# Performance work log

Measured on AMD Instinct MI355X. Metric: run time of the kernel, lower is better.

Reference implementation:

```python
import jax, jax.numpy as jnp
import numpy as np

N, E = 50000, 600000
IN_DIM, HID, HYP = 384, 128, 256
NUM_LAYERS = 3
TAU = 0.5
ALPHA = 0.1
EPS = 1e-10


def setup_inputs() -> dict:
    keys = jax.random.split(jax.random.key(0), 10)
    x = jax.random.normal(keys[0], (N, IN_DIM), dtype=jnp.float32)
    edge_index = jax.random.randint(keys[1], (2, E), 0, N, dtype=jnp.int32)
    gumbel_u = jax.random.uniform(keys[2], (N, HYP), dtype=jnp.float32, minval=1e-6, maxval=1.0 - 1e-6)
    # parameters (xavier-ish scaling)
    w_feat = jax.random.normal(keys[3], (IN_DIM, HID), dtype=jnp.float32) * np.float32(1.0 / np.sqrt(IN_DIM))
    b_feat = jnp.zeros((HID,), jnp.float32)
    w_hyper = jax.random.normal(keys[4], (HID, HYP), dtype=jnp.float32) * np.float32(np.sqrt(2.0 / (HID + HYP)))
    w_vis = jax.random.normal(keys[5], (HID, HID), dtype=jnp.float32) * np.float32(1.0 / np.sqrt(HID))
    b_vis = jnp.zeros((HID,), jnp.float32)
    w_txt = jax.random.normal(keys[6], (HID, HID), dtype=jnp.float32) * np.float32(1.0 / np.sqrt(HID))
    b_txt = jnp.zeros((HID,), jnp.float32)
    return {"x": x, "edge_index": edge_index, "gumbel_u": gumbel_u,
            "w_feat": w_feat, "b_feat": b_feat, "w_hyper": w_hyper,
            "w_vis": w_vis, "b_vis": b_vis, "w_txt": w_txt, "b_txt": b_txt}


def reference(x, edge_index, gumbel_u, w_feat, b_feat, w_hyper, w_vis, b_vis, w_txt, b_txt):
    src, dst = edge_index[0], edge_index[1]
    # LGConv gcn_norm (no self loops): deg from in-edges, norm = d_src^-1/2 * d_dst^-1/2
    deg = jax.ops.segment_sum(jnp.ones((E,), x.dtype), dst, num_segments=N)
    dinv = jnp.where(deg > 0, jnp.where(deg > 0, deg, 1.0) ** -0.5, 0.0)
    ew = dinv[src] * dinv[dst]  # [E]

    x_emb = x @ w_feat + b_feat  # [N, HID] (dropout p=0 / eval: identity)

    # stacked LightGCN propagation, mean over (num_layers+1) layer outputs
    acc = x_emb
    cur = x_emb
    for _ in range(NUM_LAYERS):
        cur = jax.ops.segment_sum(cur[src] * ew[:, None], dst, num_segments=N)
        acc = acc + cur
    local = acc / jnp.asarray(NUM_LAYERS + 1, x.dtype)

    # HGNN: gumbel-softmax soft assignment + two dense matmuls
    logits = x_emb @ w_hyper  # [N, HYP]
    g = -jnp.log(-jnp.log(gumbel_u + EPS) + EPS)
    Hm = jax.nn.softmax((logits + g) / TAU, axis=1)  # [N, HYP]
    lat = Hm.T @ x_emb            # [HYP, HID]
    hyper_out = Hm @ lat          # [N, HID]

    # F.normalize(p=2, dim=1) with eps clamp 1e-12
    nrm = jnp.maximum(jnp.linalg.norm(hyper_out, axis=1, keepdims=True), 1e-12)
    final = local + ALPHA * (hyper_out / nrm)

    x_vision = jax.nn.relu(final @ w_vis + b_vis)
    x_text = jax.nn.relu(final @ w_txt + b_txt)
    return final, x_vision, x_text
```

## Files before the change

kernel.cpp:

```cpp
#include <hip/hip_runtime.h>
#include <math.h>

#define N_NODES 50000
#define E_EDGES 600000
#define IN_DIM  384
#define HID     128
#define HYP     256

#define SCAN_NB ((N_NODES + 255) / 256)
#define EMB_NB  (N_NODES / 16)
#define DEG_NB  ((E_EDGES + 127) / 128)

typedef __attribute__((ext_vector_type(8))) short bf16x8;
typedef __attribute__((ext_vector_type(4))) float f32x4;
typedef _Float16 f16x4 __attribute__((ext_vector_type(4)));
typedef _Float16 f16x8 __attribute__((ext_vector_type(8)));

__device__ __forceinline__ unsigned short f2bf(float f) {
    unsigned u = __builtin_bit_cast(unsigned, f);
    u = (u + 0x7FFFu + ((u >> 16) & 1u)) >> 16;
    return (unsigned short)u;
}

__device__ __forceinline__ bf16x8 cvt8(float4 p, float4 q) {
    bf16x8 a;
    a[0] = (short)f2bf(p.x); a[1] = (short)f2bf(p.y);
    a[2] = (short)f2bf(p.z); a[3] = (short)f2bf(p.w);
    a[4] = (short)f2bf(q.x); a[5] = (short)f2bf(q.y);
    a[6] = (short)f2bf(q.z); a[7] = (short)f2bf(q.w);
    return a;
}

__device__ __forceinline__ bf16x8 cvt8h(f16x8 h) {
    bf16x8 a;
#pragma unroll
    for (int i = 0; i < 8; ++i) a[i] = (short)f2bf((float)h[i]);
    return a;
}


__global__ __launch_bounds__(256) void k_scan1(const int* __restrict__ deg, int* __restrict__ bsum) {
    __shared__ int sh[256];
    int tid = threadIdx.x;
    int i = blockIdx.x * 256 + tid;
    sh[tid] = (i < N_NODES) ? deg[i] : 0;
    __syncthreads();
#pragma unroll
    for (int off = 128; off > 0; off >>= 1) {
        if (tid < off) sh[tid] += sh[tid + off];
        __syncthreads();
    }
    if (tid == 0) bsum[blockIdx.x] = sh[0];
}

__global__ __launch_bounds__(256) void k_scan2(const int* __restrict__ bsum, int* __restrict__ bbase,
                                               int* __restrict__ row_start) {
    __shared__ int sh[256];
    int tid = threadIdx.x;
    int v = (tid < SCAN_NB) ? bsum[tid] : 0;
    sh[tid] = v;
    __syncthreads();
#pragma unroll
    for (int off = 1; off < 256; off <<= 1) {
        int t = (tid >= off) ? sh[tid - off] : 0;
        __syncthreads();
        sh[tid] += t;
        __syncthreads();
    }
    if (tid < SCAN_NB) bbase[tid] = sh[tid] - v;
    if (tid == 0) row_start[N_NODES] = E_EDGES;
}

__global__ __launch_bounds__(256) void k_scan3(const int* __restrict__ deg, const int* __restrict__ bbase,
                                               int* __restrict__ row_start, float* __restrict__ dinv) {
    __shared__ int sh[256];
    int tid = threadIdx.x;
    int i = blockIdx.x * 256 + tid;
    int d = (i < N_NODES) ? deg[i] : 0;
    sh[tid] = d;
    __syncthreads();
#pragma unroll
    for (int off = 1; off < 256; off <<= 1) {
        int t = (tid >= off) ? sh[tid - off] : 0;
        __syncthreads();
        sh[tid] += t;
        __syncthreads();
    }
    if (i < N_NODES) {
        row_start[i] = sh[tid] - d + bbase[blockIdx.x];
        dinv[i] = (d > 0) ? rsqrtf((float)d) : 0.0f;
    }
}

__global__ void k_fill(const int* __restrict__ src, const int* __restrict__ dst,
                       const int* __restrict__ row_start, int* __restrict__ cnt,
                       const float* __restrict__ dinv, int2* __restrict__ csr_sw) {
    int i = blockIdx.x * blockDim.x + threadIdx.x;
    if (i < E_EDGES) {
        int d = dst[i], s = src[i];
        int pos = row_start[d] + atomicAdd(&cnt[d], 1);
        csr_sw[pos] = make_int2(s, __float_as_int(dinv[s] * dinv[d]));
    }
}


__global__ __launch_bounds__(256) void k_cvt_all(const float* __restrict__ wf, const float* __restrict__ wh,
                                                 const float* __restrict__ wv, const float* __restrict__ wt,
                                                 unsigned short* __restrict__ wfT, unsigned short* __restrict__ whT,
                                                 unsigned short* __restrict__ wvT, unsigned short* __restrict__ wtT) {
    int i = blockIdx.x * 256 + threadIdx.x;
    if (i < 49152) {
        int r = i >> 7, c = i & 127;
        wfT[(size_t)c * IN_DIM + r] = f2bf(wf[i]);
    } else if (i < 49152 + 32768) {
        int j = i - 49152;
        int r = j >> 8, c = j & 255;
        whT[(size_t)c * HID + r] = f2bf(wh[j]);
    } else if (i < 49152 + 32768 + 16384) {
        int j = i - 81920;
        int r = j >> 7, c = j & 127;
        wvT[(size_t)c * HID + r] = f2bf(wv[j]);
    } else {
        int j = i - 98304;
        int r = j >> 7, c = j & 127;
        wtT[(size_t)c * HID + r] = f2bf(wt[j]);
    }
}


__global__ __launch_bounds__(128) void k_embdeg(const float* __restrict__ x, const unsigned short* __restrict__ wfT,
                                                const float* __restrict__ bf_, _Float16* __restrict__ x_embh,
                                                const int* __restrict__ dst, int* __restrict__ deg) {
    int b = blockIdx.x;
    if (b >= EMB_NB) {
        int i = (b - EMB_NB) * 128 + threadIdx.x;
        if (i < E_EDGES) atomicAdd(&deg[dst[i]], 1);
        return;
    }
    __shared__ float red[16 * HID];
    int tid = threadIdx.x;
    int wid = tid >> 6;
    int lane = tid & 63;
    int l16 = lane & 15, quad = lane >> 4;
    int m0 = b * 16;
    const float* xrow = x + (size_t)(m0 + l16) * IN_DIM + wid * 192 + quad * 8;
    float4 P[6], Q[6];
#pragma unroll
    for (int kt = 0; kt < 6; ++kt) {
        P[kt] = *reinterpret_cast<const float4*>(xrow + kt * 32);
        Q[kt] = *reinterpret_cast<const float4*>(xrow + kt * 32 + 4);
    }
    f32x4 acc[8];
#pragma unroll
    for (int nt = 0; nt < 8; ++nt) acc[nt] = (f32x4){0.f, 0.f, 0.f, 0.f};
#pragma unroll
    for (int kt = 0; kt < 6; ++kt) {
        bf16x8 a = cvt8(P[kt], Q[kt]);
#pragma unroll
        for (int nt = 0; nt < 8; ++nt) {
            bf16x8 bfr = *reinterpret_cast<const bf16x8*>(
                &wfT[(size_t)(nt * 16 + l16) * IN_DIM + wid * 192 + kt * 32 + quad * 8]);
            acc[nt] = __builtin_amdgcn_mfma_f32_16x16x32_bf16(a, bfr, acc[nt], 0, 0, 0);
        }
    }
    if (wid == 1) {
#pragma unroll
        for (int nt = 0; nt < 8; ++nt)
#pragma unroll
            for (int r = 0; r < 4; ++r)
                red[(quad * 4 + r) * HID + nt * 16 + l16] = acc[nt][r];
    }
    __syncthreads();
    if (wid == 0) {
#pragma unroll
        for (int nt = 0; nt < 8; ++nt) {
            int col = nt * 16 + l16;
            float bias = bf_[col];
#pragma unroll
            for (int r = 0; r < 4; ++r) {
                int lrow = quad * 4 + r;
                float v = acc[nt][r] + red[lrow * HID + col] + bias;
                x_embh[(size_t)(m0 + lrow) * HID + col] = (_Float16)v;
            }
        }
    }
}


__device__ __forceinline__ void fma4h(float4& a, const f16x4 v, float s) {
    a.x = fmaf((float)v.x, s, a.x);
    a.y = fmaf((float)v.y, s, a.y);
    a.z = fmaf((float)v.z, s, a.z);
    a.w = fmaf((float)v.w, s, a.w);
}

template <int INIT, int LAST>
__global__ __launch_bounds__(256) void k_prop(const _Float16* __restrict__ curh, _Float16* __restrict__ nxth,
                                              float* __restrict__ accb,
                                              const int* __restrict__ row_start,
                                              const int2* __restrict__ csr_sw) {
    int tid = threadIdx.x;
    int n = blockIdx.x * 8 + (tid >> 5);
    int c4 = (tid & 31) * 4;
    int s = row_start[n];
    int e = row_start[n + 1];
    float4 a[8];
#pragma unroll
    for (int k = 0; k < 8; ++k) a[k] = (float4){0.f, 0.f, 0.f, 0.f};
    for (int i = s; i < e; i += 8) {
        int2 pk[8];
        float wk[8];
#pragma unroll
        for (int k = 0; k < 8; ++k) {
            int j = i + k;
            pk[k] = csr_sw[(j < e) ? j : s];
            wk[k] = (j < e) ? __int_as_float(pk[k].y) : 0.0f;
        }
        f16x4 v[8];
#pragma unroll
        for (int k = 0; k < 8; ++k)
            v[k] = *reinterpret_cast<const f16x4*>(&curh[(size_t)pk[k].x * HID + c4]);
#pragma unroll
        for (int k = 0; k < 8; ++k) fma4h(a[k], v[k], wk[k]);
    }
    a[0].x += a[1].x; a[0].y += a[1].y; a[0].z += a[1].z; a[0].w += a[1].w;
    a[2].x += a[3].x; a[2].y += a[3].y; a[2].z += a[3].z; a[2].w += a[3].w;
    a[4].x += a[5].x; a[4].y += a[5].y; a[4].z += a[5].z; a[4].w += a[5].w;
    a[6].x += a[7].x; a[6].y += a[7].y; a[6].z += a[7].z; a[6].w += a[7].w;
    a[0].x += a[2].x; a[0].y += a[2].y; a[0].z += a[2].z; a[0].w += a[2].w;
    a[4].x += a[6].x; a[4].y += a[6].y; a[4].z += a[6].z; a[4].w += a[6].w;
    a[0].x += a[4].x; a[0].y += a[4].y; a[0].z += a[4].z; a[0].w += a[4].w;
    size_t o = (size_t)n * HID + c4;
    if (!LAST) {
        f16x4 oh;
        oh.x = (_Float16)a[0].x; oh.y = (_Float16)a[0].y;
        oh.z = (_Float16)a[0].z; oh.w = (_Float16)a[0].w;
        *reinterpret_cast<f16x4*>(&nxth[o]) = oh;
    }
    float4 ac;
    if (INIT) {
        f16x4 bh = *reinterpret_cast<const f16x4*>(&curh[o]);
        ac = make_float4((float)bh.x, (float)bh.y, (float)bh.z, (float)bh.w);
    } else {
        ac = *reinterpret_cast<const float4*>(&accb[o]);
    }
    ac.x += a[0].x; ac.y += a[0].y; ac.z += a[0].z; ac.w += a[0].w;
    *reinterpret_cast<float4*>(&accb[o]) = ac;
}


__global__ __launch_bounds__(64) void k_soft(const _Float16* __restrict__ x_embh,
                                             const unsigned short* __restrict__ whT,
                                             const float* __restrict__ gu, _Float16* __restrict__ Hmh) {
    int lane = threadIdx.x & 63;
    int l16 = lane & 15, quad = lane >> 4;
    int m0 = blockIdx.x * 16;
    const _Float16* xrow = x_embh + (size_t)(m0 + l16) * HID + quad * 8;
    f32x4 acc[16];
#pragma unroll
    for (int nt = 0; nt < 16; ++nt) acc[nt] = (f32x4){0.f, 0.f, 0.f, 0.f};
#pragma unroll
    for (int kt = 0; kt < HID / 32; ++kt) {
        f16x8 h = *reinterpret_cast<const f16x8*>(xrow + kt * 32);
        bf16x8 a = cvt8h(h);
#pragma unroll
        for (int nt = 0; nt < 16; ++nt) {
            bf16x8 b = *reinterpret_cast<const bf16x8*>(&whT[(size_t)(nt * 16 + l16) * HID + kt * 32 + quad * 8]);
            acc[nt] = __builtin_amdgcn_mfma_f32_16x16x32_bf16(a, b, acc[nt], 0, 0, 0);
        }
    }
#pragma unroll
    for (int nt = 0; nt < 16; ++nt) {
        int col = nt * 16 + l16;
#pragma unroll
        for (int r = 0; r < 4; ++r) {
            int row = m0 + quad * 4 + r;
            float u = gu[(size_t)row * HYP + col];
            float g = -logf(-logf(u + 1e-10f) + 1e-10f);
            acc[nt][r] = (acc[nt][r] + g) * 2.0f;
        }
    }
    float mx[4] = {-3.4e38f, -3.4e38f, -3.4e38f, -3.4e38f};
#pragma unroll
    for (int nt = 0; nt < 16; ++nt)
#pragma unroll
        for (int r = 0; r < 4; ++r) mx[r] = fmaxf(mx[r], acc[nt][r]);
#pragma unroll
    for (int r = 0; r < 4; ++r) {
        mx[r] = fmaxf(mx[r], __shfl_xor(mx[r], 1));
        mx[r] = fmaxf(mx[r], __shfl_xor(mx[r], 2));
        mx[r] = fmaxf(mx[r], __shfl_xor(mx[r], 4));
        mx[r] = fmaxf(mx[r], __shfl_xor(mx[r], 8));
    }
    float sm[4] = {0.f, 0.f, 0.f, 0.f};
#pragma unroll
    for (int nt = 0; nt < 16; ++nt)
#pragma unroll
        for (int r = 0; r < 4; ++r) {
            float e = __expf(acc[nt][r] - mx[r]);
            acc[nt][r] = e;
            sm[r] += e;
        }
#pragma unroll
    for (int r = 0; r < 4; ++r) {
        sm[r] += __shfl_xor(sm[r], 1);
        sm[r] += __shfl_xor(sm[r], 2);
        sm[r] += __shfl_xor(sm[r], 4);
        sm[r] += __shfl_xor(sm[r], 8);
        sm[r] = 1.0f / sm[r];
    }
#pragma unroll
    for (int nt = 0; nt < 16; ++nt) {
        int col = nt * 16 + l16;
#pragma unroll
        for (int r = 0; r < 4; ++r)
            Hmh[(size_t)(m0 + quad * 4 + r) * HYP + col] = (_Float16)(acc[nt][r] * sm[r]);
    }
}


#define LAT_KC 384

__global__ __launch_bounds__(256) void k_lat(const _Float16* __restrict__ Hmh, const _Float16* __restrict__ x_embh,
                                             float* __restrict__ part) {
    int htile = blockIdx.x & 1;
    int kc = blockIdx.x >> 1;
    const int chunk = (N_NODES + LAT_KC - 1) / LAT_KC;
    int start = kc * chunk;
    int end = min(N_NODES, start + chunk);
    int nn = end - start;
    int tid = threadIdx.x;
    int lh = (tid & 15) * 8;
    int d = (tid >> 4) * 8;
    const _Float16* __restrict__ hp = Hmh + (size_t)start * HYP + htile * 128 + lh;
    const _Float16* __restrict__ xp = x_embh + (size_t)start * HID + d;
    float acc[8][8];
#pragma unroll
    for (int i = 0; i < 8; ++i)
#pragma unroll
        for (int j = 0; j < 8; ++j) acc[i][j] = 0.f;
#pragma unroll 2
    for (int n = 0; n < nn; ++n) {
        f16x8 ah = *reinterpret_cast<const f16x8*>(hp);
        f16x8 bh = *reinterpret_cast<const f16x8*>(xp);
        float av[8], bv[8];
#pragma unroll
        for (int i = 0; i < 8; ++i) { av[i] = (float)ah[i]; bv[i] = (float)bh[i]; }
#pragma unroll
        for (int i = 0; i < 8; ++i)
#pragma unroll
            for (int j = 0; j < 8; ++j) acc[i][j] = fmaf(av[i], bv[j], acc[i][j]);
        hp += HYP;
        xp += HID;
    }
    float* __restrict__ pp = part + (size_t)blockIdx.x * (128 * 128) + (size_t)lh * 128 + d;
#pragma unroll
    for (int i = 0; i < 8; ++i) {
        float4 v0 = {acc[i][0], acc[i][1], acc[i][2], acc[i][3]};
        float4 v1 = {acc[i][4], acc[i][5], acc[i][6], acc[i][7]};
        *reinterpret_cast<float4*>(pp + i * 128) = v0;
        *reinterpret_cast<float4*>(pp + i * 128 + 4) = v1;
    }
}


__global__ __launch_bounds__(256) void k_lat_red(const float* __restrict__ part, unsigned short* __restrict__ latT) {
    int idx = blockIdx.x * 256 + threadIdx.x;
    int d = idx & 127;
    int h = idx >> 7;
    int htile = h >> 7;
    int lh = h & 127;
    const float* __restrict__ p0 = part + (size_t)htile * (128 * 128) + (size_t)lh * 128 + d;
    const size_t kstride = (size_t)2 * 128 * 128;
    float s0 = 0.f, s1 = 0.f, s2 = 0.f, s3 = 0.f;
#pragma unroll 4
    for (int k = 0; k < LAT_KC; k += 4) {
        s0 += p0[(size_t)k * kstride];
        s1 += p0[(size_t)(k + 1) * kstride];
        s2 += p0[(size_t)(k + 2) * kstride];
        s3 += p0[(size_t)(k + 3) * kstride];
    }
    latT[(size_t)d * HYP + h] = f2bf((s0 + s1) + (s2 + s3));
}


__global__ __launch_bounds__(64) void k_tail(const _Float16* __restrict__ Hmh, const unsigned short* __restrict__ latT,
                                             const float* __restrict__ accb,
                                             const unsigned short* __restrict__ wvT, const float* __restrict__ bv,
                                             const unsigned short* __restrict__ wtT, const float* __restrict__ bt,
                                             float* __restrict__ out_final, float* __restrict__ out_vis,
                                             float* __restrict__ out_txt) {
    __shared__ unsigned short fl[16 * HID];
    int lane = threadIdx.x & 63;
    int l16 = lane & 15, quad = lane >> 4;
    int m0 = blockIdx.x * 16;
    const _Float16* hrow = Hmh + (size_t)(m0 + l16) * HYP + quad * 8;
    f32x4 acc[8];
#pragma unroll
    for (int nt = 0; nt < 8; ++nt) acc[nt] = (f32x4){0.f, 0.f, 0.f, 0.f};
#pragma unroll
    for (int kt = 0; kt < HYP / 32; ++kt) {
        f16x8 h = *reinterpret_cast<const f16x8*>(hrow + kt * 32);
        bf16x8 a = cvt8h(h);
#pragma unroll
        for (int nt = 0; nt < 8; ++nt) {
            bf16x8 b = *reinterpret_cast<const bf16x8*>(&latT[(size_t)(nt * 16 + l16) * HYP + kt * 32 + quad * 8]);
            acc[nt] = __builtin_amdgcn_mfma_f32_16x16x32_bf16(a, b, acc[nt], 0, 0, 0);
        }
    }
    float ss[4] = {0.f, 0.f, 0.f, 0.f};
#pragma unroll
    for (int nt = 0; nt < 8; ++nt)
#pragma unroll
        for (int r = 0; r < 4; ++r) ss[r] = fmaf(acc[nt][r], acc[nt][r], ss[r]);
#pragma unroll
    for (int r = 0; r < 4; ++r) {
        ss[r] += __shfl_xor(ss[r], 1);
        ss[r] += __shfl_xor(ss[r], 2);
        ss[r] += __shfl_xor(ss[r], 4);
        ss[r] += __shfl_xor(ss[r], 8);
        ss[r] = 1.0f / fmaxf(sqrtf(ss[r]), 1e-12f);
    }
#pragma unroll
    for (int nt = 0; nt < 8; ++nt) {
        int col = nt * 16 + l16;
#pragma unroll
        for (int r = 0; r < 4; ++r) {
            int lrow = quad * 4 + r;
            size_t o = (size_t)(m0 + lrow) * HID + col;
            float f = accb[o] * 0.25f + 0.1f * (acc[nt][r] * ss[r]);
            out_final[o] = f;
            fl[lrow * HID + col] = f2bf(f);
        }
    }
    __syncthreads();
    f32x4 av[8], at4[8];
#pragma unroll
    for (int nt = 0; nt < 8; ++nt) {
        av[nt] = (f32x4){0.f, 0.f, 0.f, 0.f};
        at4[nt] = (f32x4){0.f, 0.f, 0.f, 0.f};
    }
#pragma unroll
    for (int kt = 0; kt < HID / 32; ++kt) {
        bf16x8 a = *reinterpret_cast<const bf16x8*>(&fl[l16 * HID + kt * 32 + quad * 8]);
#pragma unroll
        for (int nt = 0; nt < 8; ++nt) {
            bf16x8 b1 = *reinterpret_cast<const bf16x8*>(&wvT[(size_t)(nt * 16 + l16) * HID + kt * 32 + quad * 8]);
            bf16x8 b2 = *reinterpret_cast<const bf16x8*>(&wtT[(size_t)(nt * 16 + l16) * HID + kt * 32 + quad * 8]);
            av[nt] = __builtin_amdgcn_mfma_f32_16x16x32_bf16(a, b1, av[nt], 0, 0, 0);
            at4[nt] = __builtin_amdgcn_mfma_f32_16x16x32_bf16(a, b2, at4[nt], 0, 0, 0);
        }
    }
#pragma unroll
    for (int nt = 0; nt < 8; ++nt) {
        int col = nt * 16 + l16;
        float b1 = bv[col], b2 = bt[col];
#pragma unroll
        for (int r = 0; r < 4; ++r) {
            size_t o = (size_t)(m0 + quad * 4 + r) * HID + col;
            out_vis[o] = fmaxf(av[nt][r] + b1, 0.0f);
            out_txt[o] = fmaxf(at4[nt][r] + b2, 0.0f);
        }
    }
}


extern "C" void kernel_launch(void* const* d_in, const int* in_sizes, int n_in,
                              void* d_out, int out_size, void* d_ws, size_t ws_size,
                              hipStream_t stream) {
    const float* x      = (const float*)d_in[0];
    const int*   ei     = (const int*)d_in[1];
    const float* gu     = (const float*)d_in[2];
    const float* w_feat = (const float*)d_in[3];
    const float* b_feat = (const float*)d_in[4];
    const float* w_hyp  = (const float*)d_in[5];
    const float* w_vis  = (const float*)d_in[6];
    const float* b_vis  = (const float*)d_in[7];
    const float* w_txt  = (const float*)d_in[8];
    const float* b_txt  = (const float*)d_in[9];
    float* out = (float*)d_out;

    const int* srcv = ei;
    const int* dstv = ei + E_EDGES;

    char* p = (char*)d_ws;
    auto carve = [&p](size_t bytes) {
        char* r = p;
        p += (bytes + 63) & ~(size_t)63;
        return r;
    };
    int*      deg     = (int*)carve((size_t)N_NODES * 4);
    int*      cnt     = (int*)carve((size_t)N_NODES * 4);
    int*      rs      = (int*)carve((size_t)(N_NODES + 1) * 4);
    float*    dinv    = (float*)carve((size_t)N_NODES * 4);
    int2*     csr_sw  = (int2*)carve((size_t)E_EDGES * 8);
    _Float16* x_embh  = (_Float16*)carve((size_t)N_NODES * HID * 2);
    float*    bufA    = (float*)carve((size_t)N_NODES * HID * 4);
    float*    bufB    = (float*)carve((size_t)N_NODES * HID * 4);
    float*    accb    = (float*)carve((size_t)N_NODES * HID * 4);
    _Float16* Hmh     = (_Float16*)carve((size_t)N_NODES * HYP * 2);
    unsigned short* wfT  = (unsigned short*)carve((size_t)HID * IN_DIM * 2);
    unsigned short* whT  = (unsigned short*)carve((size_t)HYP * HID * 2);
    unsigned short* wvT  = (unsigned short*)carve((size_t)HID * HID * 2);
    unsigned short* wtT  = (unsigned short*)carve((size_t)HID * HID * 2);
    unsigned short* latT = (unsigned short*)carve((size_t)HID * HYP * 2);
    int*      bsum    = (int*)carve((size_t)SCAN_NB * 4);
    int*      bbase   = (int*)carve((size_t)SCAN_NB * 4);

    _Float16* bufAh = (_Float16*)bufA;
    _Float16* bufBh = (_Float16*)bufB;
    float* latPart = bufA;

    (void)hipMemsetAsync(d_ws, 0, (size_t)2 * N_NODES * 4 + 128, stream);

    k_cvt_all<<<448, 256, 0, stream>>>(w_feat, w_hyp, w_vis, w_txt, wfT, whT, wvT, wtT);

    k_embdeg<<<EMB_NB + DEG_NB, 128, 0, stream>>>(x, wfT, b_feat, x_embh, dstv, deg);

    k_scan1<<<SCAN_NB, 256, 0, stream>>>(deg, bsum);
    k_scan2<<<1, 256, 0, stream>>>(bsum, bbase, rs);
    k_scan3<<<SCAN_NB, 256, 0, stream>>>(deg, bbase, rs, dinv);
    k_fill<<<(E_EDGES + 255) / 256, 256, 0, stream>>>(srcv, dstv, rs, cnt, dinv, csr_sw);

    k_prop<1, 0><<<N_NODES / 8, 256, 0, stream>>>(x_embh, bufAh, accb, rs, csr_sw);
    k_prop<0, 0><<<N_NODES / 8, 256, 0, stream>>>(bufAh, bufBh, accb, rs, csr_sw);
    k_prop<0, 1><<<N_NODES / 8, 256, 0, stream>>>(bufBh, bufAh, accb, rs, csr_sw);
    k_soft<<<N_NODES / 16, 64, 0, stream>>>(x_embh, whT, gu, Hmh);
    k_lat<<<2 * LAT_KC, 256, 0, stream>>>(Hmh, x_embh, latPart);
    k_lat_red<<<(HYP * HID) / 256, 256, 0, stream>>>(latPart, latT);
    k_tail<<<N_NODES / 16, 64, 0, stream>>>(Hmh, latT, accb, wvT, b_vis, wtT, b_txt,
                                            out, out + (size_t)N_NODES * HID, out + (size_t)2 * N_NODES * HID);
}
```

Baseline: 563.7 us.

## Split embedding GEMM across column tiles with single-wave blocks, drop LDS reduction

Rewrites the x@w_feat embedding kernel so that each 64-thread block computes a 16x32 output tile over the full K=384. Previously a 128-thread block computed a 16x128 tile with K split across two waves and combined them through shared memory. This removes the LDS reduction and __syncthreads and creates four times as many blocks for more parallelism. The cost is that each x row is now read and converted to bf16 four times, once per column tile, and the degree-count blocks shrink to 64 threads.

```diff
diff --git a/kernel.cpp b/kernel.cpp
--- a/kernel.cpp
+++ b/kernel.cpp
@@ -8,8 +8,8 @@
 #define HYP     256
 
 #define SCAN_NB ((N_NODES + 255) / 256)
-#define EMB_NB  (N_NODES / 16)
-#define DEG_NB  ((E_EDGES + 127) / 128)
+#define EMB_NB  ((N_NODES / 16) * 4)
+#define DEG_NB  ((E_EDGES + 63) / 64)
 
 typedef __attribute__((ext_vector_type(8))) short bf16x8;
 typedef __attribute__((ext_vector_type(4))) float f32x4;
@@ -128,61 +128,42 @@
 }
 
 
-__global__ __launch_bounds__(128) void k_embdeg(const float* __restrict__ x, const unsigned short* __restrict__ wfT,
-                                                const float* __restrict__ bf_, _Float16* __restrict__ x_embh,
-                                                const int* __restrict__ dst, int* __restrict__ deg) {
+__global__ __launch_bounds__(64) void k_embdeg(const float* __restrict__ x, const unsigned short* __restrict__ wfT,
+                                               const float* __restrict__ bf_, _Float16* __restrict__ x_embh,
+                                               const int* __restrict__ dst, int* __restrict__ deg) {
     int b = blockIdx.x;
+    int lane = threadIdx.x;
     if (b >= EMB_NB) {
-        int i = (b - EMB_NB) * 128 + threadIdx.x;
+        int i = (b - EMB_NB) * 64 + lane;
         if (i < E_EDGES) atomicAdd(&deg[dst[i]], 1);
         return;
     }
-    __shared__ float red[16 * HID];
-    int tid = threadIdx.x;
-    int wid = tid >> 6;
-    int lane = tid & 63;
+    int ct = b & 3;
+    int m0 = (b >> 2) * 16;
+    int c0 = ct * 32;
     int l16 = lane & 15, quad = lane >> 4;
-    int m0 = b * 16;
-    const float* xrow = x + (size_t)(m0 + l16) * IN_DIM + wid * 192 + quad * 8;
-    float4 P[6], Q[6];
-#pragma unroll
-    for (int kt = 0; kt < 6; ++kt) {
-        P[kt] = *reinterpret_cast<const float4*>(xrow + kt * 32);
-        Q[kt] = *reinterpret_cast<const float4*>(xrow + kt * 32 + 4);
-    }
-    f32x4 acc[8];
-#pragma unroll
-    for (int nt = 0; nt < 8; ++nt) acc[nt] = (f32x4){0.f, 0.f, 0.f, 0.f};
-#pragma unroll
-    for (int kt = 0; kt < 6; ++kt) {
-        bf16x8 a = cvt8(P[kt], Q[kt]);
-#pragma unroll
-        for (int nt = 0; nt < 8; ++nt) {
-            bf16x8 bfr = *reinterpret_cast<const bf16x8*>(
-                &wfT[(size_t)(nt * 16 + l16) * IN_DIM + wid * 192 + kt * 32 + quad * 8]);
-            acc[nt] = __builtin_amdgcn_mfma_f32_16x16x32_bf16(a, bfr, acc[nt], 0, 0, 0);
-        }
-    }
-    if (wid == 1) {
-#pragma unroll
-        for (int nt = 0; nt < 8; ++nt)
-#pragma unroll
-            for (int r = 0; r < 4; ++r)
-                red[(quad * 4 + r) * HID + nt * 16 + l16] = acc[nt][r];
-    }
-    __syncthreads();
-    if (wid == 0) {
-#pragma unroll
-        for (int nt = 0; nt < 8; ++nt) {
-            int col = nt * 16 + l16;
-            float bias = bf_[col];
-#pragma unroll
-            for (int r = 0; r < 4; ++r) {
-                int lrow = quad * 4 + r;
-                float v = acc[nt][r] + red[lrow * HID + col] + bias;
-                x_embh[(size_t)(m0 + lrow) * HID + col] = (_Float16)v;
-            }
-        }
+    const float* xrow = x + (size_t)(m0 + l16) * IN_DIM + quad * 8;
+    const unsigned short* wp0 = wfT + (size_t)(c0 + l16) * IN_DIM + quad * 8;
+    const unsigned short* wp1 = wp0 + (size_t)16 * IN_DIM;
+    f32x4 acc0 = (f32x4){0.f, 0.f, 0.f, 0.f};
+    f32x4 acc1 = (f32x4){0.f, 0.f, 0.f, 0.f};
+#pragma unroll
+    for (int kt = 0; kt < 12; ++kt) {
+        float4 p = *reinterpret_cast<const float4*>(xrow + kt * 32);
+        float4 q = *reinterpret_cast<const float4*>(xrow + kt * 32 + 4);
+        bf16x8 a = cvt8(p, q);
+        bf16x8 b0 = *reinterpret_cast<const bf16x8*>(wp0 + kt * 32);
+        bf16x8 b1 = *reinterpret_cast<const bf16x8*>(wp1 + kt * 32);
+        acc0 = __builtin_amdgcn_mfma_f32_16x16x32_bf16(a, b0, acc0, 0, 0, 0);
+        acc1 = __builtin_amdgcn_mfma_f32_16x16x32_bf16(a, b1, acc1, 0, 0, 0);
+    }
+    float bias0 = bf_[c0 + l16];
+    float bias1 = bf_[c0 + 16 + l16];
+#pragma unroll
+    for (int r = 0; r < 4; ++r) {
+        size_t row = (size_t)(m0 + quad * 4 + r);
+        x_embh[row * HID + c0 + l16]      = (_Float16)(acc0[r] + bias0);
+        x_embh[row * HID + c0 + 16 + l16] = (_Float16)(acc1[r] + bias1);
     }
 }
 
@@ -515,7 +496,7 @@
 
     k_cvt_all<<<448, 256, 0, stream>>>(w_feat, w_hyp, w_vis, w_txt, wfT, whT, wvT, wtT);
 
-    k_embdeg<<<EMB_NB + DEG_NB, 128, 0, stream>>>(x, wfT, b_feat, x_embh, dstv, deg);
+    k_embdeg<<<EMB_NB + DEG_NB, 64, 0, stream>>>(x, wfT, b_feat, x_embh, dstv, deg);
 
     k_scan1<<<SCAN_NB, 256, 0, stream>>>(deg, bsum);
     k_scan2<<<1, 256, 0, stream>>>(bsum, bbase, rs);
```

Result: slower. 579.1 us (+2.7%).
